# Performance work log

Measured on AMD Instinct MI355X. Metric: run time of the kernel, lower is better.

Reference implementation:

```python
import jax, jax.numpy as jnp
import numpy as np

N, D, T = 4096, 512, 4096
TEMPERATURE = 0.07
MARGIN = 0.5
CONT_WEIGHT = 1.0
TRIP_WEIGHT = 0.3
EPS = 1e-8        # eps in the log / denominator (matches torch code)
PD_EPS = 1e-6     # F.pairwise_distance default eps added to the difference


def setup_inputs() -> dict:
    key = jax.random.key(0)
    k1, k2, k3 = jax.random.split(key, 3)
    embeddings = jax.random.normal(k1, (N, D), dtype=jnp.float32)
    labels = jax.random.randint(k2, (N,), 0, 256)            # ~16 positives per place
    triplets = jax.random.randint(k3, (T, 3), 0, N)          # (anchor, pos, neg) indices
    return {"embeddings": embeddings, "labels": labels, "triplets": triplets}


def reference(embeddings, labels, triplets):
    # ---- MultiPositiveContrastiveLoss ----
    # F.cosine_similarity normalizes each row with eps=1e-8 on the norm.
    norms = jnp.linalg.norm(embeddings, axis=1, keepdims=True)
    n_emb = embeddings / jnp.maximum(norms, EPS)
    sim = (n_emb @ n_emb.T) / TEMPERATURE                    # [N, N]

    pos_mask = (labels[:, None] == labels[None, :]).astype(embeddings.dtype)
    pos_mask = pos_mask * (1.0 - jnp.eye(sim.shape[0], dtype=embeddings.dtype))

    exp_sim = jnp.exp(sim)
    pos_sum = (exp_sim * pos_mask).sum(axis=1)
    total_sum = exp_sim.sum(axis=1)
    loss = -jnp.log(pos_sum / (total_sum + EPS) + EPS)

    valid = pos_mask.sum(axis=1) > 0
    cnt = valid.sum()
    cont_loss = jnp.where(
        cnt > 0,
        jnp.where(valid, loss, 0.0).sum() / jnp.maximum(cnt, 1).astype(loss.dtype),
        jnp.zeros((), loss.dtype),
    )

    # ---- TripletLoss, vectorized over all triplets (replaces Python loop) ----
    a = embeddings[triplets[:, 0]]   # [T, D]
    p = embeddings[triplets[:, 1]]
    ng = embeddings[triplets[:, 2]]
    pos_dist = jnp.linalg.norm(a - p + PD_EPS, axis=1)
    neg_dist = jnp.linalg.norm(a - ng + PD_EPS, axis=1)
    trip_loss = jnp.maximum(pos_dist - neg_dist + MARGIN, 0.0).mean()

    total = CONT_WEIGHT * cont_loss + TRIP_WEIGHT * trip_loss
    return (total, cont_loss, trip_loss)
```

## Files before the change

### kernel.cpp

```cpp
#include <hip/hip_runtime.h>

#define NN 4096
#define DD 512
#define TT 4096

typedef __bf16 bf16x8 __attribute__((ext_vector_type(8)));
typedef float f32x4 __attribute__((ext_vector_type(4)));

constexpr float INV_TEMP = 1.0f / 0.07f;

#define AS1(p) ((__attribute__((address_space(1))) const void*)(p))
#define AS3(p) ((__attribute__((address_space(3))) void*)(p))

__global__ __launch_bounds__(256) void k_normtrip(const float* __restrict__ emb,
                                                  __bf16* __restrict__ nemb,
                                                  const int* __restrict__ trip,
                                                  float* __restrict__ tl) {
    int wave = threadIdx.x >> 6, lane = threadIdx.x & 63;
    int row = blockIdx.x * 4 + wave;

    int ia = trip[row * 3 + 0], ip = trip[row * 3 + 1], ig = trip[row * 3 + 2];
    const float4* pa = (const float4*)(emb + (size_t)ia * DD);
    const float4* pp = (const float4*)(emb + (size_t)ip * DD);
    const float4* pn = (const float4*)(emb + (size_t)ig * DD);
    float d1 = 0.0f, d2 = 0.0f;
    #pragma unroll
    for (int j = 0; j < 2; ++j) {
        float4 a = pa[lane * 2 + j];
        float4 p = pp[lane * 2 + j];
        float4 n = pn[lane * 2 + j];
        float dx;
        dx = a.x - p.x + 1e-6f; d1 += dx * dx;
        dx = a.y - p.y + 1e-6f; d1 += dx * dx;
        dx = a.z - p.z + 1e-6f; d1 += dx * dx;
        dx = a.w - p.w + 1e-6f; d1 += dx * dx;
        dx = a.x - n.x + 1e-6f; d2 += dx * dx;
        dx = a.y - n.y + 1e-6f; d2 += dx * dx;
        dx = a.z - n.z + 1e-6f; d2 += dx * dx;
        dx = a.w - n.w + 1e-6f; d2 += dx * dx;
    }

    const float4* src = (const float4*)(emb + (size_t)row * DD);
    float4 x0 = src[lane * 2 + 0];
    float4 x1 = src[lane * 2 + 1];
    float ss = x0.x * x0.x + x0.y * x0.y + x0.z * x0.z + x0.w * x0.w +
               x1.x * x1.x + x1.y * x1.y + x1.z * x1.z + x1.w * x1.w;
    #pragma unroll
    for (int m = 1; m < 64; m <<= 1) ss += __shfl_xor(ss, m, 64);
    float inv = 1.0f / fmaxf(sqrtf(ss), 1e-8f);
    bf16x8 v;
    v[0] = (__bf16)(x0.x * inv); v[1] = (__bf16)(x0.y * inv);
    v[2] = (__bf16)(x0.z * inv); v[3] = (__bf16)(x0.w * inv);
    v[4] = (__bf16)(x1.x * inv); v[5] = (__bf16)(x1.y * inv);
    v[6] = (__bf16)(x1.z * inv); v[7] = (__bf16)(x1.w * inv);
    *(bf16x8*)(nemb + (size_t)row * DD + lane * 8) = v;

    #pragma unroll
    for (int m = 1; m < 64; m <<= 1) {
        d1 += __shfl_xor(d1, m, 64);
        d2 += __shfl_xor(d2, m, 64);
    }
    if (lane == 0) tl[row] = fmaxf(sqrtf(d1) - sqrtf(d2) + 0.5f, 0.0f);
}


#define VMW(N) asm volatile("s_waitcnt vmcnt(" #N ")" ::: "memory")
#define NOVM ((void)0)

#define STAGE_A(T, H) do { \
    __builtin_amdgcn_global_load_lds(AS1(gA0 + (size_t)((H) * 128) * DD + (T) * 64), \
                                     AS3(lA0 + (((T) & 1) * 2 + (H)) * 8192), 16, 0, 0); \
    __builtin_amdgcn_global_load_lds(AS1(gA0 + (size_t)((H) * 128 + 8) * DD + (T) * 64), \
                                     AS3(lA0 + (((T) & 1) * 2 + (H)) * 8192 + 512), 16, 0, 0); \
} while (0)

#define STAGE_B(T, H) do { \
    __builtin_amdgcn_global_load_lds(AS1(gB0 + (size_t)((H) * 128) * DD + (T) * 64), \
                                     AS3(lB0 + (((T) & 1) * 2 + (H)) * 8192), 16, 0, 0); \
    __builtin_amdgcn_global_load_lds(AS1(gB0 + (size_t)((H) * 128 + 8) * DD + (T) * 64), \
                                     AS3(lB0 + (((T) & 1) * 2 + (H)) * 8192 + 512), 16, 0, 0); \
} while (0)

#define PHASE(PAR, LOADA, QM, QN, STAGE_STMT, VM_STMT) do { \
    const __bf16* aB_ = aSm + ((PAR) * 2 + (QM)) * 8192; \
    const __bf16* bB_ = bSm + ((PAR) * 2 + (QN)) * 8192; \
    if (LOADA) { \
        _Pragma("unroll") \
        for (int fm_ = 0; fm_ < 4; ++fm_) { \
            af[fm_][0] = *(const bf16x8*)(aB_ + fm_ * 1024 + rdA0); \
            af[fm_][1] = *(const bf16x8*)(aB_ + fm_ * 1024 + rdA1); \
        } \
    } \
    _Pragma("unroll") \
    for (int fn_ = 0; fn_ < 2; ++fn_) { \
        bfr[fn_][0] = *(const bf16x8*)(bB_ + fn_ * 1024 + rdB0); \
        bfr[fn_][1] = *(const bf16x8*)(bB_ + fn_ * 1024 + rdB1); \
    } \
    STAGE_STMT; \
    asm volatile("s_waitcnt lgkmcnt(0)" ::: "memory"); \
    __builtin_amdgcn_sched_barrier(0); \
    __builtin_amdgcn_s_setprio(1); \
    _Pragma("unroll") \
    for (int kc_ = 0; kc_ < 2; ++kc_) { \
        _Pragma("unroll") \
        for (int fm_ = 0; fm_ < 4; ++fm_) { \
            _Pragma("unroll") \
            for (int fn_ = 0; fn_ < 2; ++fn_) \
                acc[QM][QN][fm_][fn_] = __builtin_amdgcn_mfma_f32_16x16x32_bf16( \
                    af[fm_][kc_], bfr[fn_][kc_], acc[QM][QN][fm_][fn_], 0, 0, 0); \
        } \
    } \
    __builtin_amdgcn_s_setprio(0); \
    __builtin_amdgcn_sched_barrier(0); \
    VM_STMT; \
    asm volatile("" ::: "memory"); \
    __builtin_amdgcn_s_barrier(); \
} while (0)

#define GROUP(G, S12, S34, VM1, VM4) do { \
    PHASE((G) & 1, 1, 0, 0, { if (S12) STAGE_A((G) + 1, 1); }, VM1); \
    PHASE((G) & 1, 0, 0, 1, { if (S12) STAGE_B((G) + 1, 1); }, NOVM); \
    PHASE((G) & 1, 1, 1, 0, { if (S34) STAGE_A((G) + 2, 0); }, NOVM); \
    PHASE((G) & 1, 0, 1, 1, { if (S34) STAGE_B((G) + 2, 0); }, VM4); \
} while (0)

__global__ __launch_bounds__(512, 2) void k_contrast(const __bf16* __restrict__ nemb,
                                                     const int* __restrict__ labels,
                                                     float* __restrict__ posP,
                                                     float* __restrict__ totP) {
    __shared__ __attribute__((aligned(16))) __bf16 aSm[4 * 8192];
    __shared__ __attribute__((aligned(16))) __bf16 bSm[4 * 8192];
    __shared__ int rlab[256];
    __shared__ int clab[256];

    int tid = threadIdx.x;
    int lane = tid & 63, wave = tid >> 6;
    int wr = wave >> 2, wc = wave & 3;
    int l15 = lane & 15, quad = lane >> 4;
    int swz = l15 & 7;

    int bid = blockIdx.x;
    int xcd = bid & 7, idx = bid >> 3;
    int rowblk = (xcd >> 1) * 4 + (idx >> 3);
    int colblk = (xcd & 1) * 8 + (idx & 7);
    int row0 = rowblk * 256, col0 = colblk * 256;

    if (tid < 256) rlab[tid] = labels[row0 + tid];
    else           clab[tid - 256] = labels[col0 + tid - 256];

    int srow = wave * 16 + ((tid >> 3) & 7);
    int scol = ((tid & 7) ^ ((tid >> 3) & 7)) * 8;
    const __bf16* gA0 = nemb + (size_t)(row0 + srow) * DD + scol;
    const __bf16* gB0 = nemb + (size_t)(col0 + srow) * DD + scol;
    __bf16* lA0 = aSm + wave * 1024 + (tid & 63) * 8;
    __bf16* lB0 = bSm + wave * 1024 + (tid & 63) * 8;

    int rdA0 = (wr * 64 + l15) * 64 + ((quad ^ swz) * 8);
    int rdA1 = (wr * 64 + l15) * 64 + (((4 + quad) ^ swz) * 8);
    int rdB0 = (wc * 32 + l15) * 64 + ((quad ^ swz) * 8);
    int rdB1 = (wc * 32 + l15) * 64 + (((4 + quad) ^ swz) * 8);

    f32x4 acc[2][2][4][2];
    #pragma unroll
    for (int a = 0; a < 2; ++a)
        #pragma unroll
        for (int b = 0; b < 2; ++b)
            #pragma unroll
            for (int c = 0; c < 4; ++c)
                #pragma unroll
                for (int d = 0; d < 2; ++d) {
                    f32x4 z = {0.0f, 0.0f, 0.0f, 0.0f};
                    acc[a][b][c][d] = z;
                }

    bf16x8 af[4][2], bfr[2][2];

    STAGE_A(0, 0); STAGE_B(0, 0);
    STAGE_A(0, 1); STAGE_B(0, 1);
    STAGE_A(1, 0); STAGE_B(1, 0);
    VMW(8);
    asm volatile("" ::: "memory");
    __builtin_amdgcn_s_barrier();

    GROUP(0, 1, 1, VMW(6), VMW(8));
    GROUP(1, 1, 1, VMW(6), VMW(8));
    GROUP(2, 1, 1, VMW(6), VMW(8));
    GROUP(3, 1, 1, VMW(6), VMW(8));
    GROUP(4, 1, 1, VMW(6), VMW(8));
    GROUP(5, 1, 1, VMW(6), VMW(8));
    GROUP(6, 1, 0, VMW(6), VMW(4));
    GROUP(7, 0, 0, VMW(0), NOVM);

    #pragma unroll
    for (int qm = 0; qm < 2; ++qm)
    #pragma unroll
    for (int fm = 0; fm < 4; ++fm) {
        int rloc = qm * 128 + wr * 64 + fm * 16 + quad * 4;
        int gibase = row0 + rloc;
        int rl[4];
        #pragma unroll
        for (int v = 0; v < 4; ++v) rl[v] = rlab[rloc + v];
        float tv[4] = {0, 0, 0, 0}, pv[4] = {0, 0, 0, 0};
        #pragma unroll
        for (int qn = 0; qn < 2; ++qn)
        #pragma unroll
        for (int fn = 0; fn < 2; ++fn) {
            int cloc = qn * 128 + wc * 32 + fn * 16 + l15;
            int cl = clab[cloc];
            int gj = col0 + cloc;
            f32x4 a = acc[qm][qn][fm][fn];
            #pragma unroll
            for (int v = 0; v < 4; ++v) {
                float e = __expf(a[v] * INV_TEMP);
                tv[v] += e;
                bool match = (rl[v] == cl) && ((gibase + v) != gj);
                pv[v] += match ? e : 0.0f;
            }
        }
        #pragma unroll
        for (int m = 1; m < 16; m <<= 1) {
            #pragma unroll
            for (int v = 0; v < 4; ++v) {
                tv[v] += __shfl_xor(tv[v], m, 64);
                pv[v] += __shfl_xor(pv[v], m, 64);
            }
        }
        if (l15 == 0) {
            #pragma unroll
            for (int v = 0; v < 4; ++v) {
                int o = (gibase + v) * 64 + colblk * 4 + wc;
                posP[o] = pv[v];
                totP[o] = tv[v];
            }
        }
    }
}

__global__ __launch_bounds__(256) void k_rowloss(const float* __restrict__ posP,
                                                 const float* __restrict__ totP,
                                                 const int* __restrict__ labels,
                                                 float* __restrict__ rloss,
                                                 float* __restrict__ rvalid) {
    __shared__ int hist[256];
    int tid = threadIdx.x;
    hist[tid] = 0;
    __syncthreads();
    #pragma unroll
    for (int j = 0; j < 16; ++j)
        atomicAdd(&hist[labels[tid + j * 256]], 1);
    __syncthreads();

    int wave = tid >> 6, lane = tid & 63;
    int row = blockIdx.x * 4 + wave;
    float p = posP[row * 64 + lane];
    float t = totP[row * 64 + lane];
    #pragma unroll
    for (int m = 1; m < 64; m <<= 1) {
        p += __shfl_xor(p, m, 64);
        t += __shfl_xor(t, m, 64);
    }
    if (lane == 0) {
        bool valid = hist[labels[row]] > 1;
        float loss = valid ? -logf(p / (t + 1e-8f) + 1e-8f) : 0.0f;
        rloss[row] = loss;
        rvalid[row] = valid ? 1.0f : 0.0f;
    }
}

__global__ __launch_bounds__(256) void k_final(const float* __restrict__ rloss,
                                               const float* __restrict__ rvalid,
                                               const float* __restrict__ tl,
                                               float* __restrict__ out) {
    int tid = threadIdx.x;
    float sl = 0.0f, sv = 0.0f, st = 0.0f;
    for (int i = tid; i < NN; i += 256) {
        sl += rloss[i];
        sv += rvalid[i];
        st += tl[i];
    }
    #pragma unroll
    for (int m = 1; m < 64; m <<= 1) {
        sl += __shfl_xor(sl, m, 64);
        sv += __shfl_xor(sv, m, 64);
        st += __shfl_xor(st, m, 64);
    }
    __shared__ float red[3][4];
    int lane = tid & 63, wave = tid >> 6;
    if (lane == 0) { red[0][wave] = sl; red[1][wave] = sv; red[2][wave] = st; }
    __syncthreads();
    if (tid == 0) {
        float SL = red[0][0] + red[0][1] + red[0][2] + red[0][3];
        float SV = red[1][0] + red[1][1] + red[1][2] + red[1][3];
        float ST = red[2][0] + red[2][1] + red[2][2] + red[2][3];
        float cont = (SV > 0.0f) ? (SL / SV) : 0.0f;
        float trip = ST * (1.0f / (float)TT);
        out[0] = cont + 0.3f * trip;
        out[1] = cont;
        out[2] = trip;
    }
}

extern "C" void kernel_launch(void* const* d_in, const int* in_sizes, int n_in,
                              void* d_out, int out_size, void* d_ws, size_t ws_size,
                              hipStream_t stream) {
    const float* emb = (const float*)d_in[0];
    const int* labels = (const int*)d_in[1];
    const int* trips = (const int*)d_in[2];
    float* out = (float*)d_out;
    char* ws = (char*)d_ws;

    __bf16* nemb  = (__bf16*)(ws);
    float* posP   = (float*)(ws + 4194304);
    float* totP   = (float*)(ws + 5242880);
    float* rloss  = (float*)(ws + 6291456);
    float* rvalid = (float*)(ws + 6307840);
    float* tl     = (float*)(ws + 6324224);

    k_normtrip<<<NN / 4, 256, 0, stream>>>(emb, nemb, trips, tl);
    k_contrast<<<256, 512, 0, stream>>>(nemb, labels, posP, totP);
    k_rowloss<<<NN / 4, 256, 0, stream>>>(posP, totP, labels, rloss, rvalid);
    k_final<<<1, 256, 0, stream>>>(rloss, rvalid, tl, out);
}
```

Before: 100.3 us.

## Replace phased 4-quadrant GEMM pipeline with simple double-buffered K loop

Replaces the hand-scheduled GEMM mainloop in the contrastive kernel. The old loop split the 256x256 tile into quadrants, used fine-grained vmcnt waits, setprio and sched_barrier. The new loop is a plain double-buffered loop over 64-wide K slices, with each wave owning a 128x64 sub-tile and a __syncthreads per slice. This is simpler and gives more MFMA work per LDS read phase, but it drops the finer overlap and the explicit wait control. That risks load stalls, since the barrier does not by itself wait on the asynchronous global-to-LDS loads.

```diff
diff --git a/kernel.cpp b/kernel.cpp
--- a/kernel.cpp
+++ b/kernel.cpp
@@ -64,72 +64,12 @@
 }
 
 
-#define VMW(N) asm volatile("s_waitcnt vmcnt(" #N ")" ::: "memory")
-#define NOVM ((void)0)
-
-#define STAGE_A(T, H) do { \
-    __builtin_amdgcn_global_load_lds(AS1(gA0 + (size_t)((H) * 128) * DD + (T) * 64), \
-                                     AS3(lA0 + (((T) & 1) * 2 + (H)) * 8192), 16, 0, 0); \
-    __builtin_amdgcn_global_load_lds(AS1(gA0 + (size_t)((H) * 128 + 8) * DD + (T) * 64), \
-                                     AS3(lA0 + (((T) & 1) * 2 + (H)) * 8192 + 512), 16, 0, 0); \
-} while (0)
-
-#define STAGE_B(T, H) do { \
-    __builtin_amdgcn_global_load_lds(AS1(gB0 + (size_t)((H) * 128) * DD + (T) * 64), \
-                                     AS3(lB0 + (((T) & 1) * 2 + (H)) * 8192), 16, 0, 0); \
-    __builtin_amdgcn_global_load_lds(AS1(gB0 + (size_t)((H) * 128 + 8) * DD + (T) * 64), \
-                                     AS3(lB0 + (((T) & 1) * 2 + (H)) * 8192 + 512), 16, 0, 0); \
-} while (0)
-
-#define PHASE(PAR, LOADA, QM, QN, STAGE_STMT, VM_STMT) do { \
-    const __bf16* aB_ = aSm + ((PAR) * 2 + (QM)) * 8192; \
-    const __bf16* bB_ = bSm + ((PAR) * 2 + (QN)) * 8192; \
-    if (LOADA) { \
-        _Pragma("unroll") \
-        for (int fm_ = 0; fm_ < 4; ++fm_) { \
-            af[fm_][0] = *(const bf16x8*)(aB_ + fm_ * 1024 + rdA0); \
-            af[fm_][1] = *(const bf16x8*)(aB_ + fm_ * 1024 + rdA1); \
-        } \
-    } \
-    _Pragma("unroll") \
-    for (int fn_ = 0; fn_ < 2; ++fn_) { \
-        bfr[fn_][0] = *(const bf16x8*)(bB_ + fn_ * 1024 + rdB0); \
-        bfr[fn_][1] = *(const bf16x8*)(bB_ + fn_ * 1024 + rdB1); \
-    } \
-    STAGE_STMT; \
-    asm volatile("s_waitcnt lgkmcnt(0)" ::: "memory"); \
-    __builtin_amdgcn_sched_barrier(0); \
-    __builtin_amdgcn_s_setprio(1); \
-    _Pragma("unroll") \
-    for (int kc_ = 0; kc_ < 2; ++kc_) { \
-        _Pragma("unroll") \
-        for (int fm_ = 0; fm_ < 4; ++fm_) { \
-            _Pragma("unroll") \
-            for (int fn_ = 0; fn_ < 2; ++fn_) \
-                acc[QM][QN][fm_][fn_] = __builtin_amdgcn_mfma_f32_16x16x32_bf16( \
-                    af[fm_][kc_], bfr[fn_][kc_], acc[QM][QN][fm_][fn_], 0, 0, 0); \
-        } \
-    } \
-    __builtin_amdgcn_s_setprio(0); \
-    __builtin_amdgcn_sched_barrier(0); \
-    VM_STMT; \
-    asm volatile("" ::: "memory"); \
-    __builtin_amdgcn_s_barrier(); \
-} while (0)
-
-#define GROUP(G, S12, S34, VM1, VM4) do { \
-    PHASE((G) & 1, 1, 0, 0, { if (S12) STAGE_A((G) + 1, 1); }, VM1); \
-    PHASE((G) & 1, 0, 0, 1, { if (S12) STAGE_B((G) + 1, 1); }, NOVM); \
-    PHASE((G) & 1, 1, 1, 0, { if (S34) STAGE_A((G) + 2, 0); }, NOVM); \
-    PHASE((G) & 1, 0, 1, 1, { if (S34) STAGE_B((G) + 2, 0); }, VM4); \
-} while (0)
-
 __global__ __launch_bounds__(512, 2) void k_contrast(const __bf16* __restrict__ nemb,
                                                      const int* __restrict__ labels,
                                                      float* __restrict__ posP,
                                                      float* __restrict__ totP) {
-    __shared__ __attribute__((aligned(16))) __bf16 aSm[4 * 8192];
-    __shared__ __attribute__((aligned(16))) __bf16 bSm[4 * 8192];
+    __shared__ __attribute__((aligned(16))) __bf16 aS[2][256 * 64];
+    __shared__ __attribute__((aligned(16))) __bf16 bS[2][256 * 64];
     __shared__ int rlab[256];
     __shared__ int clab[256];
 
@@ -148,67 +88,77 @@
     if (tid < 256) rlab[tid] = labels[row0 + tid];
     else           clab[tid - 256] = labels[col0 + tid - 256];
 
-    int srow = wave * 16 + ((tid >> 3) & 7);
-    int scol = ((tid & 7) ^ ((tid >> 3) & 7)) * 8;
-    const __bf16* gA0 = nemb + (size_t)(row0 + srow) * DD + scol;
-    const __bf16* gB0 = nemb + (size_t)(col0 + srow) * DD + scol;
-    __bf16* lA0 = aSm + wave * 1024 + (tid & 63) * 8;
-    __bf16* lB0 = bSm + wave * 1024 + (tid & 63) * 8;
-
-    int rdA0 = (wr * 64 + l15) * 64 + ((quad ^ swz) * 8);
-    int rdA1 = (wr * 64 + l15) * 64 + (((4 + quad) ^ swz) * 8);
-    int rdB0 = (wc * 32 + l15) * 64 + ((quad ^ swz) * 8);
-    int rdB1 = (wc * 32 + l15) * 64 + (((4 + quad) ^ swz) * 8);
-
-    f32x4 acc[2][2][4][2];
-    #pragma unroll
-    for (int a = 0; a < 2; ++a)
-        #pragma unroll
-        for (int b = 0; b < 2; ++b)
-            #pragma unroll
-            for (int c = 0; c < 4; ++c)
+    int srr = (tid >> 3) & 7;
+    int scol = ((tid & 7) ^ srr) * 8;
+    const __bf16* gA0 = nemb + (size_t)(row0 + wave * 32 + srr) * DD + scol;
+    const __bf16* gB0 = nemb + (size_t)(col0 + wave * 32 + srr) * DD + scol;
+    int ldst = wave * 2048 + (tid & 63) * 8;
+
+    f32x4 acc[8][4];
+    #pragma unroll
+    for (int fm = 0; fm < 8; ++fm)
+        #pragma unroll
+        for (int fn = 0; fn < 4; ++fn) {
+            f32x4 z = {0.0f, 0.0f, 0.0f, 0.0f};
+            acc[fm][fn] = z;
+        }
+
+    #pragma unroll
+    for (int j = 0; j < 4; ++j) {
+        __builtin_amdgcn_global_load_lds(AS1(gA0 + (size_t)(j * 8) * DD),
+                                         AS3(&aS[0][ldst + j * 512]), 16, 0, 0);
+        __builtin_amdgcn_global_load_lds(AS1(gB0 + (size_t)(j * 8) * DD),
+                                         AS3(&bS[0][ldst + j * 512]), 16, 0, 0);
+    }
+    __syncthreads();
+
+    #pragma unroll
+    for (int kt = 0; kt < 8; ++kt) {
+        int cur = kt & 1;
+        if (kt < 7) {
+            #pragma unroll
+            for (int j = 0; j < 4; ++j) {
+                __builtin_amdgcn_global_load_lds(AS1(gA0 + (size_t)(j * 8) * DD + (kt + 1) * 64),
+                                                 AS3(&aS[cur ^ 1][ldst + j * 512]), 16, 0, 0);
+                __builtin_amdgcn_global_load_lds(AS1(gB0 + (size_t)(j * 8) * DD + (kt + 1) * 64),
+                                                 AS3(&bS[cur ^ 1][ldst + j * 512]), 16, 0, 0);
+            }
+        }
+        #pragma unroll
+        for (int kc = 0; kc < 2; ++kc) {
+            bf16x8 af[8], bf[4];
+            #pragma unroll
+            for (int fm = 0; fm < 8; ++fm)
+                af[fm] = *(const bf16x8*)(&aS[cur][(wr * 128 + fm * 16 + l15) * 64 +
+                                                   (((kc * 4 + quad) ^ swz) * 8)]);
+            #pragma unroll
+            for (int fn = 0; fn < 4; ++fn)
+                bf[fn] = *(const bf16x8*)(&bS[cur][(wc * 64 + fn * 16 + l15) * 64 +
+                                                   (((kc * 4 + quad) ^ swz) * 8)]);
+            #pragma unroll
+            for (int fm = 0; fm < 8; ++fm)
                 #pragma unroll
-                for (int d = 0; d < 2; ++d) {
-                    f32x4 z = {0.0f, 0.0f, 0.0f, 0.0f};
-                    acc[a][b][c][d] = z;
-                }
-
-    bf16x8 af[4][2], bfr[2][2];
-
-    STAGE_A(0, 0); STAGE_B(0, 0);
-    STAGE_A(0, 1); STAGE_B(0, 1);
-    STAGE_A(1, 0); STAGE_B(1, 0);
-    VMW(8);
-    asm volatile("" ::: "memory");
-    __builtin_amdgcn_s_barrier();
-
-    GROUP(0, 1, 1, VMW(6), VMW(8));
-    GROUP(1, 1, 1, VMW(6), VMW(8));
-    GROUP(2, 1, 1, VMW(6), VMW(8));
-    GROUP(3, 1, 1, VMW(6), VMW(8));
-    GROUP(4, 1, 1, VMW(6), VMW(8));
-    GROUP(5, 1, 1, VMW(6), VMW(8));
-    GROUP(6, 1, 0, VMW(6), VMW(4));
-    GROUP(7, 0, 0, VMW(0), NOVM);
-
-    #pragma unroll
-    for (int qm = 0; qm < 2; ++qm)
-    #pragma unroll
-    for (int fm = 0; fm < 4; ++fm) {
-        int rloc = qm * 128 + wr * 64 + fm * 16 + quad * 4;
+                for (int fn = 0; fn < 4; ++fn)
+                    acc[fm][fn] = __builtin_amdgcn_mfma_f32_16x16x32_bf16(
+                        af[fm], bf[fn], acc[fm][fn], 0, 0, 0);
+        }
+        __syncthreads();
+    }
+
+    #pragma unroll
+    for (int fm = 0; fm < 8; ++fm) {
+        int rloc = wr * 128 + fm * 16 + quad * 4;
         int gibase = row0 + rloc;
         int rl[4];
         #pragma unroll
         for (int v = 0; v < 4; ++v) rl[v] = rlab[rloc + v];
         float tv[4] = {0, 0, 0, 0}, pv[4] = {0, 0, 0, 0};
         #pragma unroll
-        for (int qn = 0; qn < 2; ++qn)
-        #pragma unroll
-        for (int fn = 0; fn < 2; ++fn) {
-            int cloc = qn * 128 + wc * 32 + fn * 16 + l15;
+        for (int fn = 0; fn < 4; ++fn) {
+            int cloc = wc * 64 + fn * 16 + l15;
             int cl = clab[cloc];
             int gj = col0 + cloc;
-            f32x4 a = acc[qm][qn][fm][fn];
+            f32x4 a = acc[fm][fn];
             #pragma unroll
             for (int v = 0; v < 4; ++v) {
                 float e = __expf(a[v] * INV_TEMP);
```

Result: slower. 103.7 us (+3.4%).
